# Optimization experiments

Measured on AMD Instinct MI355X. Metric: run time of the kernel, lower is better.

Reference implementation:

```python
import jax, jax.numpy as jnp
import numpy as np

NUM_NODES = 256
IN_FEAT = 64
HIDDEN = 512
N_CLASSES = 2
BATCH = 256


def setup_inputs() -> dict:
    key = jax.random.key(0)
    ks = jax.random.split(key, 10)
    return {
        "z": jax.random.normal(ks[0], (BATCH, 1, NUM_NODES, NUM_NODES), dtype=jnp.float32),
        "node_emb": jax.random.normal(ks[1], (NUM_NODES, IN_FEAT), dtype=jnp.float32),
        "w1": jax.random.normal(ks[2], (IN_FEAT, HIDDEN), dtype=jnp.float32) * (1.0 / np.sqrt(IN_FEAT)),
        "b1": jnp.zeros((HIDDEN,), dtype=jnp.float32),
        "w2": jax.random.normal(ks[3], (HIDDEN, HIDDEN), dtype=jnp.float32) * (1.0 / np.sqrt(HIDDEN)),
        "b2": jnp.zeros((HIDDEN,), dtype=jnp.float32),
        "w3": jax.random.normal(ks[4], (HIDDEN, HIDDEN), dtype=jnp.float32) * (1.0 / np.sqrt(HIDDEN)),
        "b3": jnp.zeros((HIDDEN,), dtype=jnp.float32),
        "fcw": jax.random.normal(ks[5], (HIDDEN, N_CLASSES), dtype=jnp.float32) * (1.0 / np.sqrt(HIDDEN)),
        "fcb": jnp.zeros((N_CLASSES,), dtype=jnp.float32),
    }


def reference(z, node_emb, w1, b1, w2, b2, w3, b3, fcw, fcb):
    # z: (B, 1, N, N) latent interpreted as weighted adjacency
    z_sq = jnp.squeeze(z, axis=1)                         # (B, N, N)
    A = jax.nn.sigmoid(z_sq)
    A = (A + jnp.swapaxes(A, 1, 2)) * 0.5                  # symmetrize
    A_hat = A + jnp.eye(A.shape[-1], dtype=A.dtype)[None]  # add self loops
    D_hat = jnp.sum(A_hat, axis=2) + 1e-6                  # (B, N) degrees
    d_inv_sqrt = D_hat ** -0.5
    # norm_A = D^{-1/2} A_hat D^{-1/2} via row/col scaling (same math as diag bmm)
    norm_A = A_hat * d_inv_sqrt[:, :, None] * d_inv_sqrt[:, None, :]

    X = jnp.broadcast_to(node_emb[None], (z.shape[0],) + node_emb.shape)  # (B, N, F)
    H1 = jax.nn.relu(jnp.einsum('bij,bjh->bih', norm_A, X @ w1 + b1))
    H2 = jax.nn.relu(jnp.einsum('bij,bjh->bih', norm_A, H1 @ w2 + b2))
    H3 = jax.nn.relu(jnp.einsum('bij,bjh->bih', norm_A, H2 @ w3 + b3))
    graph_emb = jnp.mean(H3, axis=1)                       # (B, H)
    logits = graph_emb @ fcw + fcb                         # (B, n_classes)
    return logits
```

## Files before the change

kernel.cpp:

```cpp
#include <hip/hip_runtime.h>
#include <stdint.h>

#define B_ 256
#define N_ 256
#define F_ 64
#define H_ 512

typedef _Float16 f16;
typedef _Float16 f16x8 __attribute__((ext_vector_type(8)));
typedef _Float16 f16x4 __attribute__((ext_vector_type(4)));
typedef _Float16 f16x2 __attribute__((ext_vector_type(2)));
typedef float    f32x4 __attribute__((ext_vector_type(4)));

__device__ __forceinline__ float sigmoidf_(float x) {
    return 1.0f / (1.0f + __expf(-x));
}

#define BAR_ACQ(N) do { \
    asm volatile("s_waitcnt vmcnt(" #N ")" ::: "memory"); \
    __builtin_amdgcn_s_barrier(); \
    __builtin_amdgcn_sched_barrier(0); } while (0)
#define BAR_REL() do { \
    __builtin_amdgcn_sched_barrier(0); \
    __builtin_amdgcn_s_barrier(); } while (0)

__global__ __launch_bounds__(512) void k_fsum(const float* __restrict__ z,
                                              f16* __restrict__ nA) {
    __shared__ f16 T[256 * 256];
    __shared__ float cpart[8][256];
    __shared__ float rpart[256][2];
    __shared__ float Dv[256];

    const int b = blockIdx.x;
    const int tid = threadIdx.x, lane = tid & 63, w = tid >> 6;
    const float* zb = z + (size_t)b * (N_ * N_);

    auto swz = [](int i) { return (i & 31) ^ (i >> 5); };

    float colacc[4] = {0.f, 0.f, 0.f, 0.f};
    const int ch = lane >> 1, half = lane & 1;
    for (int r = 0; r < 32; r++) {
        int i = w * 32 + r;
        float4 v = *(const float4*)(zb + (size_t)i * N_ + lane * 4);
        float s0 = sigmoidf_(v.x), s1 = sigmoidf_(v.y),
              s2 = sigmoidf_(v.z), s3 = sigmoidf_(v.w);
        f16x4 sv = { (f16)s0, (f16)s1, (f16)s2, (f16)s3 };
        *(f16x4*)&T[i * 256 + ((ch ^ swz(i)) << 3) + half * 4] = sv;
        colacc[0] += s0; colacc[1] += s1; colacc[2] += s2; colacc[3] += s3;
    }
    #pragma unroll
    for (int k = 0; k < 4; k++) cpart[w][lane * 4 + k] = colacc[k];
    __syncthreads();

    {
        int i = tid >> 1, h = tid & 1;
        float s = 0.f;
        #pragma unroll
        for (int c = 0; c < 16; c++) {
            int cc = h * 16 + c;
            f16x8 v = *(const f16x8*)&T[i * 256 + ((cc ^ swz(i)) << 3)];
            #pragma unroll
            for (int k = 0; k < 8; k++) s += (float)v[k];
        }
        rpart[i][h] = s;
    }
    __syncthreads();

    if (tid < 256) {
        float cs = 0.f;
        #pragma unroll
        for (int ww = 0; ww < 8; ww++) cs += cpart[ww][tid];
        float rs = rpart[tid][0] + rpart[tid][1];
        Dv[tid] = rsqrtf(1.0f + 1e-6f + 0.5f * (rs + cs));
    }
    __syncthreads();

    f16* Ob = nA + (size_t)b * (N_ * N_);
    #pragma unroll
    for (int tt = 0; tt < 2; tt++) {
        int tile = tt * 512 + tid;
        int I = tile >> 5, J = tile & 31;
        f16x8 a[8], bm[8];
        #pragma unroll
        for (int r = 0; r < 8; r++) {
            int ia = I * 8 + r;
            a[r] = *(const f16x8*)&T[ia * 256 + ((J ^ swz(ia)) << 3)];
        }
        #pragma unroll
        for (int r = 0; r < 8; r++) {
            int jb = J * 8 + r;
            bm[r] = *(const f16x8*)&T[jb * 256 + ((I ^ swz(jb)) << 3)];
        }
        float dj[8];
        #pragma unroll
        for (int k = 0; k < 8; k++) dj[k] = Dv[J * 8 + k];
        #pragma unroll
        for (int r = 0; r < 8; r++) {
            float di = Dv[I * 8 + r];
            f16x8 o;
            #pragma unroll
            for (int k = 0; k < 8; k++) {
                float v = 0.5f * ((float)a[r][k] + (float)bm[k][r]);
                if (I * 8 + r == J * 8 + k) v += 1.0f;
                o[k] = (f16)(v * di * dj[k]);
            }
            *(f16x8*)&Ob[(size_t)(I * 8 + r) * N_ + J * 8] = o;
        }
    }
}

__global__ __launch_bounds__(256) void k_prep(const float* __restrict__ ne,
                                              const float* __restrict__ w1,
                                              const float* __restrict__ b1,
                                              const float* __restrict__ w2,
                                              const float* __restrict__ w3,
                                              f16* __restrict__ XW1t,
                                              f16* __restrict__ w2t,
                                              f16* __restrict__ w3t) {
    int bid = blockIdx.x;
    if (bid < 512) {
        int h = bid, node = threadIdx.x;
        float s = b1[h];
        #pragma unroll 8
        for (int k = 0; k < F_; k++) s += ne[node * F_ + k] * w1[k * H_ + h];
        XW1t[h * N_ + node] = (f16)s;
    } else {
        int idx4 = bid - 512;
        int which = idx4 >> 10;
        const float* src = which ? w3 : w2;
        f16* dst = which ? w3t : w2t;
        int idx = (idx4 & 1023) * 256 + threadIdx.x;
        int k = idx >> 9, n = idx & 511;
        dst[n * H_ + k] = (f16)src[k * H_ + n];
    }
}

template <int KDIM, int MODE>
__global__ __launch_bounds__(256, 4) void k_gemm(const f16* __restrict__ A, long aBatch,
                                                 const f16* __restrict__ Bt, long bBatch,
                                                 f16* __restrict__ Out,
                                                 const float* __restrict__ bias,
                                                 float* __restrict__ gp) {
    __shared__ f16 As[128 * 64];
    __shared__ f16 Bs[128 * 64];
    const int tid  = threadIdx.x;
    const int lane = tid & 63, wave = tid >> 6;
    const int wm = wave >> 1, wn = wave & 1;

    const int lin = blockIdx.x;
    const int xcd = lin & 7, q = lin >> 3;
    const int n_t = q & 3, p = q >> 2;
    const int grp = xcd * 64 + p;
    const int b   = grp >> 1, m_t = grp & 1;
    const int m0 = m_t * 128, n0 = n_t * 128;

    const f16* Ab = A + (size_t)b * aBatch;
    const f16* Bb = Bt + (size_t)b * bBatch;

    f32x4 acc[4][4];
    #pragma unroll
    for (int i = 0; i < 4; i++)
        #pragma unroll
        for (int j = 0; j < 4; j++)
            #pragma unroll
            for (int r = 0; r < 4; r++) acc[i][j][r] = 0.0f;

    const int lr = lane >> 3;
    const int kc = (lane & 7) ^ lr;
    const int ln15 = lane & 15;

    for (int kk = 0; kk < KDIM; kk += 64) {
        #pragma unroll
        for (int c = 0; c < 4; c++) {
            int chunk = wave * 4 + c;
            int row = chunk * 8 + lr;
            __builtin_amdgcn_global_load_lds(
                (__attribute__((address_space(1))) void*)(Ab + (size_t)(m0 + row) * KDIM + kk + kc * 8),
                (__attribute__((address_space(3))) void*)(&As[chunk * 512]), 16, 0, 0);
            __builtin_amdgcn_global_load_lds(
                (__attribute__((address_space(1))) void*)(Bb + (size_t)(n0 + row) * KDIM + kk + kc * 8),
                (__attribute__((address_space(3))) void*)(&Bs[chunk * 512]), 16, 0, 0);
        }
        __syncthreads();

        #pragma unroll
        for (int ks = 0; ks < 2; ks++) {
            const int rkc = ks * 4 + (lane >> 4);
            f16x8 aF[4];
            #pragma unroll
            for (int t = 0; t < 4; t++) {
                int ra = wm * 64 + t * 16 + ln15;
                aF[t] = *(const f16x8*)&As[(ra * 8 + (rkc ^ (ra & 7))) * 8];
            }
            #pragma unroll
            for (int h2 = 0; h2 < 2; h2++) {
                f16x8 bF[2];
                #pragma unroll
                for (int t = 0; t < 2; t++) {
                    int rb = wn * 64 + (h2 * 2 + t) * 16 + ln15;
                    bF[t] = *(const f16x8*)&Bs[(rb * 8 + (rkc ^ (rb & 7))) * 8];
                }
                #pragma unroll
                for (int mt = 0; mt < 4; mt++)
                    #pragma unroll
                    for (int t = 0; t < 2; t++)
                        acc[mt][h2 * 2 + t] = __builtin_amdgcn_mfma_f32_16x16x32_f16(aF[mt], bF[t], acc[mt][h2 * 2 + t], 0, 0, 0);
            }
        }
        __syncthreads();
    }

    const int quad = lane >> 4;
    if (MODE == 0) {
        f16* Ob = Out + (size_t)b * (N_ * H_);
        #pragma unroll
        for (int mt = 0; mt < 4; mt++) {
            int node = m0 + wm * 64 + mt * 16 + quad * 4;
            #pragma unroll
            for (int nt = 0; nt < 4; nt++) {
                int h = n0 + wn * 64 + nt * 16 + ln15;
                #pragma unroll
                for (int rr = 0; rr < 4; rr++) {
                    float v = acc[mt][nt][rr];
                    v = v > 0.f ? v : 0.f;
                    Ob[(size_t)(node + rr) * H_ + h] = (f16)v;
                }
            }
        }
    }
}

template <int REDUCE>
__global__ __launch_bounds__(1024, 4) void k_fused(const f16* __restrict__ Hin,
                                                   const f16* __restrict__ Wt,
                                                   const float* __restrict__ bias,
                                                   const f16* __restrict__ nA,
                                                   f16* __restrict__ Hout,
                                                   float* __restrict__ gp) {
    __shared__ f16 As[2][16384];
    __shared__ f16 WU[32768];

    const int tid  = threadIdx.x;
    const int lane = tid & 63, wave = tid >> 6;
    const int ln15 = lane & 15, quad = lane >> 4;
    const int wm = wave >> 2, wn = wave & 3;

    const int lin = blockIdx.x;
    const int xcd = lin & 7, p = lin >> 3;
    const int grp = xcd * 128 + p;
    const int b = grp >> 2, hc = grp & 3;

    const f16* Hb = Hin + (size_t)b * (N_ * H_);
    const f16* Ab = nA + (size_t)b * (N_ * N_);
    const f16* Wc = Wt + (size_t)(hc * 128) * H_;

    const int lr = lane >> 3;
    const int kc = (lane & 7) ^ lr;

    auto stage1 = [&](int buf, int kt) {
        #pragma unroll
        for (int c = 0; c < 2; c++) {
            int chunk = wave * 2 + c;
            int row = chunk * 8 + lr;
            __builtin_amdgcn_global_load_lds(
                (__attribute__((address_space(1))) void*)(Hb + (size_t)row * H_ + kt * 64 + kc * 8),
                (__attribute__((address_space(3))) void*)(&As[buf][chunk * 512]), 16, 0, 0);
        }
        {
            int chunk = wave;
            int row = chunk * 8 + lr;
            __builtin_amdgcn_global_load_lds(
                (__attribute__((address_space(1))) void*)(Wc + (size_t)row * H_ + kt * 64 + kc * 8),
                (__attribute__((address_space(3))) void*)(&WU[buf * 8192 + chunk * 512]), 16, 0, 0);
        }
    };
    auto stage2 = [&](int buf, int jt) {
        #pragma unroll
        for (int c = 0; c < 2; c++) {
            int chunk = wave * 2 + c;
            int row = chunk * 8 + lr;
            __builtin_amdgcn_global_load_lds(
                (__attribute__((address_space(1))) void*)(Ab + (size_t)row * N_ + jt * 64 + kc * 8),
                (__attribute__((address_space(3))) void*)(&As[buf][chunk * 512]), 16, 0, 0);
        }
    };

    f32x4 acc[4][2];
    #pragma unroll
    for (int i = 0; i < 4; i++)
        #pragma unroll
        for (int j = 0; j < 2; j++)
            #pragma unroll
            for (int r = 0; r < 4; r++) acc[i][j][r] = 0.0f;

    stage1(0, 0);
    for (int kt = 0; kt < 8; ++kt) {
        const int buf = kt & 1;
        if (kt < 7) {
            stage1(buf ^ 1, kt + 1);
            BAR_ACQ(3);
        } else {
            stage2(0, 0);
            BAR_ACQ(2);
        }
        __builtin_amdgcn_s_setprio(1);
        #pragma unroll
        for (int ks = 0; ks < 2; ks++) {
            const int rkc = ks * 4 + quad;
            f16x8 aF[4], bF[2];
            #pragma unroll
            for (int t = 0; t < 4; t++) {
                int ra = wm * 64 + t * 16 + ln15;
                aF[t] = *(const f16x8*)&As[buf][(ra * 8 + (rkc ^ (ra & 7))) * 8];
            }
            #pragma unroll
            for (int t = 0; t < 2; t++) {
                int rb = wn * 32 + t * 16 + ln15;
                bF[t] = *(const f16x8*)&WU[buf * 8192 + (rb * 8 + (rkc ^ (rb & 7))) * 8];
            }
            #pragma unroll
            for (int mt = 0; mt < 4; mt++)
                #pragma unroll
                for (int nt = 0; nt < 2; nt++)
                    acc[mt][nt] = __builtin_amdgcn_mfma_f32_16x16x32_f16(aF[mt], bF[nt], acc[mt][nt], 0, 0, 0);
        }
        __builtin_amdgcn_s_setprio(0);
        BAR_REL();
    }

    #pragma unroll
    for (int nt = 0; nt < 2; nt++) {
        int hl = wn * 32 + nt * 16 + ln15;
        float bv = bias[hc * 128 + hl];
        #pragma unroll
        for (int mt = 0; mt < 4; mt++) {
            int j = wm * 64 + mt * 16 + quad * 4;
            int slot = (j >> 3) ^ (hl & 7);
            f16x4 v;
            #pragma unroll
            for (int rr = 0; rr < 4; rr++) v[rr] = (f16)(acc[mt][nt][rr] + bv);
            *(f16x4*)&WU[hl * 256 + slot * 8 + (j & 7)] = v;
        }
    }
    asm volatile("s_waitcnt lgkmcnt(0)" ::: "memory");
    __builtin_amdgcn_s_barrier();
    __builtin_amdgcn_sched_barrier(0);

    #pragma unroll
    for (int i = 0; i < 4; i++)
        #pragma unroll
        for (int j = 0; j < 2; j++)
            #pragma unroll
            for (int r = 0; r < 4; r++) acc[i][j][r] = 0.0f;

    for (int jt = 0; jt < 4; ++jt) {
        const int buf = jt & 1;
        if (jt < 3) {
            stage2(buf ^ 1, jt + 1);
            BAR_ACQ(2);
        } else {
            BAR_ACQ(0);
        }
        __builtin_amdgcn_s_setprio(1);
        #pragma unroll
        for (int ks = 0; ks < 2; ks++) {
            const int rkc = ks * 4 + quad;
            f16x8 aF[4], bF[2];
            #pragma unroll
            for (int t = 0; t < 4; t++) {
                int ra = wm * 64 + t * 16 + ln15;
                aF[t] = *(const f16x8*)&As[buf][(ra * 8 + (rkc ^ (ra & 7))) * 8];
            }
            #pragma unroll
            for (int t = 0; t < 2; t++) {
                int rb = wn * 32 + t * 16 + ln15;
                int g = jt * 8 + rkc;
                bF[t] = *(const f16x8*)&WU[rb * 256 + ((g ^ (rb & 7)) * 8)];
            }
            #pragma unroll
            for (int mt = 0; mt < 4; mt++)
                #pragma unroll
                for (int nt = 0; nt < 2; nt++)
                    acc[mt][nt] = __builtin_amdgcn_mfma_f32_16x16x32_f16(aF[mt], bF[nt], acc[mt][nt], 0, 0, 0);
        }
        __builtin_amdgcn_s_setprio(0);
        BAR_REL();
    }

    if (REDUCE == 0) {
        f16* Ob = Hout + (size_t)b * (N_ * H_);
        #pragma unroll
        for (int mt = 0; mt < 4; mt++) {
            int node = wm * 64 + mt * 16 + quad * 4;
            #pragma unroll
            for (int nt = 0; nt < 2; nt++) {
                int hg = hc * 128 + wn * 32 + nt * 16 + ln15;
                #pragma unroll
                for (int rr = 0; rr < 4; rr++) {
                    float v = acc[mt][nt][rr];
                    v = v > 0.f ? v : 0.f;
                    Ob[(size_t)(node + rr) * H_ + hg] = (f16)v;
                }
            }
        }
    } else {
        float part[2];
        #pragma unroll
        for (int nt = 0; nt < 2; nt++) {
            float s = 0.f;
            #pragma unroll
            for (int mt = 0; mt < 4; mt++)
                #pragma unroll
                for (int rr = 0; rr < 4; rr++) {
                    float v = acc[mt][nt][rr];
                    s += (v > 0.f ? v : 0.f);
                }
            s += __shfl_down(s, 32, 64);
            s += __shfl_down(s, 16, 64);
            part[nt] = s;
        }
        __syncthreads();
        float* red = (float*)&As[0][0];
        if (quad == 0) {
            #pragma unroll
            for (int nt = 0; nt < 2; nt++)
                red[wave * 32 + nt * 16 + ln15] = part[nt];
        }
        __syncthreads();
        if (tid < 128) {
            int wnl = tid >> 5, cl = tid & 31;
            float g = red[(0 * 4 + wnl) * 32 + cl] + red[(1 * 4 + wnl) * 32 + cl]
                    + red[(2 * 4 + wnl) * 32 + cl] + red[(3 * 4 + wnl) * 32 + cl];
            gp[(size_t)b * H_ + hc * 128 + tid] = g;
        }
    }
}

__global__ __launch_bounds__(256) void k_logits(const float* __restrict__ gp,
                                                const float* __restrict__ fcw,
                                                const float* __restrict__ fcb,
                                                float* __restrict__ out) {
    int b = blockIdx.x, tid = threadIdx.x;
    const float* g = gp + (size_t)b * H_;
    float g0 = g[tid];
    float g1 = g[tid + 256];
    float p0 = g0 * fcw[tid * 2 + 0] + g1 * fcw[(tid + 256) * 2 + 0];
    float p1 = g0 * fcw[tid * 2 + 1] + g1 * fcw[(tid + 256) * 2 + 1];
    for (int off = 32; off; off >>= 1) {
        p0 += __shfl_down(p0, off, 64);
        p1 += __shfl_down(p1, off, 64);
    }
    __shared__ float r0[4], r1[4];
    int lane = tid & 63, w = tid >> 6;
    if (lane == 0) { r0[w] = p0; r1[w] = p1; }
    __syncthreads();
    const float inv = 1.0f / N_;
    if (tid == 0) out[b * 2 + 0] = (r0[0] + r0[1] + r0[2] + r0[3]) * inv + fcb[0];
    if (tid == 1) out[b * 2 + 1] = (r1[0] + r1[1] + r1[2] + r1[3]) * inv + fcb[1];
}

extern "C" void kernel_launch(void* const* d_in, const int* in_sizes, int n_in,
                              void* d_out, int out_size, void* d_ws, size_t ws_size,
                              hipStream_t stream) {
    const float* z   = (const float*)d_in[0];
    const float* ne  = (const float*)d_in[1];
    const float* w1  = (const float*)d_in[2];
    const float* b1  = (const float*)d_in[3];
    const float* w2  = (const float*)d_in[4];
    const float* b2  = (const float*)d_in[5];
    const float* w3  = (const float*)d_in[6];
    const float* b3  = (const float*)d_in[7];
    const float* fcw = (const float*)d_in[8];
    const float* fcb = (const float*)d_in[9];
    float* out = (float*)d_out;

    char* ws = (char*)d_ws;
    f16*   T     = (f16*)(ws + 0);
    f16*   nA    = (f16*)(ws + 67108864);
    f16*   Hh    = (f16*)(ws + 100663296);
    float* gpart = (float*)(ws + 100663296);
    f16*   XW1t  = (f16*)(ws + 167772160);
    f16*   w2t   = (f16*)(ws + 168034304);
    f16*   w3t   = (f16*)(ws + 168558592);

    k_fsum<<<256, 512, 0, stream>>>(z, nA);
    k_prep<<<2560, 256, 0, stream>>>(ne, w1, b1, w2, w3, XW1t, w2t, w3t);

    k_gemm<256, 0><<<2048, 256, 0, stream>>>(nA, 65536, XW1t, 0, Hh, nullptr, nullptr);
    k_fused<0><<<1024, 1024, 0, stream>>>(Hh, w2t, b2, nA, T, nullptr);
    k_fused<1><<<1024, 1024, 0, stream>>>(T, w3t, b3, nA, nullptr, gpart);

    k_logits<<<B_, 256, 0, stream>>>(gpart, fcw, fcb, out);
}
```

Measured before the change: 293.2 us.

## Fuse first GCN aggregation GEMM into adjacency normalization kernel

The normalized adjacency is now written back into the block's shared-memory tile, and that tile is used directly as the A operand of an MFMA GEMM against XW1t to produce H1 within the same kernel. This removes the separate k_gemm launch and its re-read of nA from global memory. Normalization now runs over only the lower-triangular 8x8 tile pairs and writes each mirrored tile from registers, which halves the shared-memory loads. The tradeoffs are that k_prep must run before k_fsum, and that only 256 blocks of 512 threads perform the first layer's GEMM, with B fragments read straight from global memory and no staging.

Result: slower. 383.0 us (+30.6%).

```diff
diff --git a/kernel.cpp b/kernel.cpp
--- a/kernel.cpp
+++ b/kernel.cpp
@@ -25,7 +25,9 @@
     __builtin_amdgcn_s_barrier(); } while (0)
 
 __global__ __launch_bounds__(512) void k_fsum(const float* __restrict__ z,
-                                              f16* __restrict__ nA) {
+                                              const f16* __restrict__ XW1t,
+                                              f16* __restrict__ nA,
+                                              f16* __restrict__ H1) {
     __shared__ f16 T[256 * 256];
     __shared__ float cpart[8][256];
     __shared__ float rpart[256][2];
@@ -65,7 +67,6 @@
         rpart[i][h] = s;
     }
     __syncthreads();
-
     if (tid < 256) {
         float cs = 0.f;
         #pragma unroll
@@ -76,10 +77,14 @@
     __syncthreads();
 
     f16* Ob = nA + (size_t)b * (N_ * N_);
-    #pragma unroll
-    for (int tt = 0; tt < 2; tt++) {
-        int tile = tt * 512 + tid;
-        int I = tile >> 5, J = tile & 31;
+    for (int pp = 0; pp < 2; pp++) {
+        if (pp == 1 && tid >= 16) break;
+        int p = pp * 512 + tid;
+        int I = (int)((sqrtf(8.0f * (float)p + 1.0f) - 1.0f) * 0.5f);
+        while (I * (I + 1) / 2 > p) I--;
+        while ((I + 1) * (I + 2) / 2 <= p) I++;
+        int J = p - I * (I + 1) / 2;
+
         f16x8 a[8], bm[8];
         #pragma unroll
         for (int r = 0; r < 8; r++) {
@@ -91,20 +96,88 @@
             int jb = J * 8 + r;
             bm[r] = *(const f16x8*)&T[jb * 256 + ((I ^ swz(jb)) << 3)];
         }
-        float dj[8];
-        #pragma unroll
-        for (int k = 0; k < 8; k++) dj[k] = Dv[J * 8 + k];
+        float di[8], dj[8];
+        #pragma unroll
+        for (int k = 0; k < 8; k++) { di[k] = Dv[I * 8 + k]; dj[k] = Dv[J * 8 + k]; }
+
+        f16x8 o[8];
         #pragma unroll
         for (int r = 0; r < 8; r++) {
-            float di = Dv[I * 8 + r];
-            f16x8 o;
             #pragma unroll
             for (int k = 0; k < 8; k++) {
                 float v = 0.5f * ((float)a[r][k] + (float)bm[k][r]);
-                if (I * 8 + r == J * 8 + k) v += 1.0f;
-                o[k] = (f16)(v * di * dj[k]);
-            }
-            *(f16x8*)&Ob[(size_t)(I * 8 + r) * N_ + J * 8] = o;
+                if (I == J && r == k) v += 1.0f;
+                o[r][k] = (f16)(v * di[r] * dj[k]);
+            }
+        }
+        #pragma unroll
+        for (int r = 0; r < 8; r++) {
+            int ia = I * 8 + r;
+            *(f16x8*)&Ob[(size_t)ia * N_ + J * 8] = o[r];
+            *(f16x8*)&T[ia * 256 + ((J ^ swz(ia)) << 3)] = o[r];
+        }
+        if (I != J) {
+            #pragma unroll
+            for (int r = 0; r < 8; r++) {
+                int jb = J * 8 + r;
+                f16x8 om;
+                #pragma unroll
+                for (int k = 0; k < 8; k++) om[k] = o[k][r];
+                *(f16x8*)&Ob[(size_t)jb * N_ + I * 8] = om;
+                *(f16x8*)&T[jb * 256 + ((I ^ swz(jb)) << 3)] = om;
+            }
+        }
+    }
+    __syncthreads();
+
+    const int ln15 = lane & 15, quad = lane >> 4;
+    const int wm = w >> 1, wn = w & 1;
+    f16* Hb = H1 + (size_t)b * (N_ * H_);
+    for (int no = 0; no < 4; no++) {
+        const int n0 = (wn * 4 + no) * 64;
+        f32x4 acc[4][4];
+        #pragma unroll
+        for (int i = 0; i < 4; i++)
+            #pragma unroll
+            for (int j = 0; j < 4; j++)
+                #pragma unroll
+                for (int r = 0; r < 4; r++) acc[i][j][r] = 0.0f;
+
+        for (int kk = 0; kk < 4; kk++) {
+            #pragma unroll
+            for (int ks = 0; ks < 2; ks++) {
+                const int g = kk * 8 + ks * 4 + quad;
+                f16x8 aF[4], bF[4];
+                #pragma unroll
+                for (int t = 0; t < 4; t++) {
+                    int i = wm * 64 + t * 16 + ln15;
+                    aF[t] = *(const f16x8*)&T[i * 256 + ((g ^ swz(i)) << 3)];
+                }
+                #pragma unroll
+                for (int t = 0; t < 4; t++) {
+                    int h = n0 + t * 16 + ln15;
+                    bF[t] = *(const f16x8*)&XW1t[(size_t)h * 256 + g * 8];
+                }
+                #pragma unroll
+                for (int mt = 0; mt < 4; mt++)
+                    #pragma unroll
+                    for (int nt = 0; nt < 4; nt++)
+                        acc[mt][nt] = __builtin_amdgcn_mfma_f32_16x16x32_f16(aF[mt], bF[nt], acc[mt][nt], 0, 0, 0);
+            }
+        }
+        #pragma unroll
+        for (int mt = 0; mt < 4; mt++) {
+            int node = wm * 64 + mt * 16 + quad * 4;
+            #pragma unroll
+            for (int nt = 0; nt < 4; nt++) {
+                int h = n0 + nt * 16 + ln15;
+                #pragma unroll
+                for (int rr = 0; rr < 4; rr++) {
+                    float v = acc[mt][nt][rr];
+                    v = v > 0.f ? v : 0.f;
+                    Hb[(size_t)(node + rr) * H_ + h] = (f16)v;
+                }
+            }
         }
     }
 }
@@ -135,101 +208,6 @@
     }
 }
 
-template <int KDIM, int MODE>
-__global__ __launch_bounds__(256, 4) void k_gemm(const f16* __restrict__ A, long aBatch,
-                                                 const f16* __restrict__ Bt, long bBatch,
-                                                 f16* __restrict__ Out,
-                                                 const float* __restrict__ bias,
-                                                 float* __restrict__ gp) {
-    __shared__ f16 As[128 * 64];
-    __shared__ f16 Bs[128 * 64];
-    const int tid  = threadIdx.x;
-    const int lane = tid & 63, wave = tid >> 6;
-    const int wm = wave >> 1, wn = wave & 1;
-
-    const int lin = blockIdx.x;
-    const int xcd = lin & 7, q = lin >> 3;
-    const int n_t = q & 3, p = q >> 2;
-    const int grp = xcd * 64 + p;
-    const int b   = grp >> 1, m_t = grp & 1;
-    const int m0 = m_t * 128, n0 = n_t * 128;
-
-    const f16* Ab = A + (size_t)b * aBatch;
-    const f16* Bb = Bt + (size_t)b * bBatch;
-
-    f32x4 acc[4][4];
-    #pragma unroll
-    for (int i = 0; i < 4; i++)
-        #pragma unroll
-        for (int j = 0; j < 4; j++)
-            #pragma unroll
-            for (int r = 0; r < 4; r++) acc[i][j][r] = 0.0f;
-
-    const int lr = lane >> 3;
-    const int kc = (lane & 7) ^ lr;
-    const int ln15 = lane & 15;
-
-    for (int kk = 0; kk < KDIM; kk += 64) {
-        #pragma unroll
-        for (int c = 0; c < 4; c++) {
-            int chunk = wave * 4 + c;
-            int row = chunk * 8 + lr;
-            __builtin_amdgcn_global_load_lds(
-                (__attribute__((address_space(1))) void*)(Ab + (size_t)(m0 + row) * KDIM + kk + kc * 8),
-                (__attribute__((address_space(3))) void*)(&As[chunk * 512]), 16, 0, 0);
-            __builtin_amdgcn_global_load_lds(
-                (__attribute__((address_space(1))) void*)(Bb + (size_t)(n0 + row) * KDIM + kk + kc * 8),
-                (__attribute__((address_space(3))) void*)(&Bs[chunk * 512]), 16, 0, 0);
-        }
-        __syncthreads();
-
-        #pragma unroll
-        for (int ks = 0; ks < 2; ks++) {
-            const int rkc = ks * 4 + (lane >> 4);
-            f16x8 aF[4];
-            #pragma unroll
-            for (int t = 0; t < 4; t++) {
-                int ra = wm * 64 + t * 16 + ln15;
-                aF[t] = *(const f16x8*)&As[(ra * 8 + (rkc ^ (ra & 7))) * 8];
-            }
-            #pragma unroll
-            for (int h2 = 0; h2 < 2; h2++) {
-                f16x8 bF[2];
-                #pragma unroll
-                for (int t = 0; t < 2; t++) {
-                    int rb = wn * 64 + (h2 * 2 + t) * 16 + ln15;
-                    bF[t] = *(const f16x8*)&Bs[(rb * 8 + (rkc ^ (rb & 7))) * 8];
-                }
-                #pragma unroll
-                for (int mt = 0; mt < 4; mt++)
-                    #pragma unroll
-                    for (int t = 0; t < 2; t++)
-                        acc[mt][h2 * 2 + t] = __builtin_amdgcn_mfma_f32_16x16x32_f16(aF[mt], bF[t], acc[mt][h2 * 2 + t], 0, 0, 0);
-            }
-        }
-        __syncthreads();
-    }
-
-    const int quad = lane >> 4;
-    if (MODE == 0) {
-        f16* Ob = Out + (size_t)b * (N_ * H_);
-        #pragma unroll
-        for (int mt = 0; mt < 4; mt++) {
-            int node = m0 + wm * 64 + mt * 16 + quad * 4;
-            #pragma unroll
-            for (int nt = 0; nt < 4; nt++) {
-                int h = n0 + wn * 64 + nt * 16 + ln15;
-                #pragma unroll
-                for (int rr = 0; rr < 4; rr++) {
-                    float v = acc[mt][nt][rr];
-                    v = v > 0.f ? v : 0.f;
-                    Ob[(size_t)(node + rr) * H_ + h] = (f16)v;
-                }
-            }
-        }
-    }
-}
-
 template <int REDUCE>
 __global__ __launch_bounds__(1024, 4) void k_fused(const f16* __restrict__ Hin,
                                                    const f16* __restrict__ Wt,
@@ -483,10 +461,9 @@
     f16*   w2t   = (f16*)(ws + 168034304);
     f16*   w3t   = (f16*)(ws + 168558592);
 
-    k_fsum<<<256, 512, 0, stream>>>(z, nA);
     k_prep<<<2560, 256, 0, stream>>>(ne, w1, b1, w2, w3, XW1t, w2t, w3t);
-
-    k_gemm<256, 0><<<2048, 256, 0, stream>>>(nA, 65536, XW1t, 0, Hh, nullptr, nullptr);
+    k_fsum<<<256, 512, 0, stream>>>(z, XW1t, nA, Hh);
+
     k_fused<0><<<1024, 1024, 0, stream>>>(Hh, w2t, b2, nA, T, nullptr);
     k_fused<1><<<1024, 1024, 0, stream>>>(T, w3t, b3, nA, nullptr, gpart);
 
```

## Replace layer-1 GEMM with double-buffered 1024-thread kernel computing full hidden width

Applied to the files above, without the earlier changes.

The first aggregation GEMM (norm_A times XW1) is rewritten so each 1024-thread block handles one 128-node tile across all 512 hidden features in two passes. This replaces four 256-thread blocks that each reloaded the same A tile. Global-to-LDS loads are double-buffered with explicit waitcnt barriers and raised wave priority around the MFMA section. The operands are swapped so output writes become vectorized 4-wide f16 stores. The intent is to cut redundant A traffic and hide load latency, at the cost of fewer, larger blocks and more LDS per block.

Result: slower. 301.9 us (+3.0%).

```diff
diff --git a/kernel.cpp b/kernel.cpp
--- a/kernel.cpp
+++ b/kernel.cpp
@@ -135,99 +135,117 @@
     }
 }
 
-template <int KDIM, int MODE>
-__global__ __launch_bounds__(256, 4) void k_gemm(const f16* __restrict__ A, long aBatch,
-                                                 const f16* __restrict__ Bt, long bBatch,
-                                                 f16* __restrict__ Out,
-                                                 const float* __restrict__ bias,
-                                                 float* __restrict__ gp) {
-    __shared__ f16 As[128 * 64];
-    __shared__ f16 Bs[128 * 64];
-    const int tid  = threadIdx.x;
+__global__ __launch_bounds__(1024, 4) void k_gemm2(const f16* __restrict__ nA,
+                                                   const f16* __restrict__ XW1t,
+                                                   f16* __restrict__ H1) {
+    __shared__ f16 Bs[2][16384];
+    __shared__ f16 Am[2][8192];
+
+    const int tid = threadIdx.x;
     const int lane = tid & 63, wave = tid >> 6;
-    const int wm = wave >> 1, wn = wave & 1;
+    const int ln15 = lane & 15, quad = lane >> 4;
+    const int wm = wave >> 2, wn = wave & 3;
 
     const int lin = blockIdx.x;
-    const int xcd = lin & 7, q = lin >> 3;
-    const int n_t = q & 3, p = q >> 2;
+    const int xcd = lin & 7, p = lin >> 3;
     const int grp = xcd * 64 + p;
-    const int b   = grp >> 1, m_t = grp & 1;
-    const int m0 = m_t * 128, n0 = n_t * 128;
-
-    const f16* Ab = A + (size_t)b * aBatch;
-    const f16* Bb = Bt + (size_t)b * bBatch;
-
-    f32x4 acc[4][4];
+    const int b = grp >> 1, m_t = grp & 1;
+    const int m0 = m_t * 128;
+
+    const f16* Ab = nA + (size_t)b * (N_ * N_);
+    f16* Hb = H1 + (size_t)b * (N_ * H_);
+
+    const int lr = lane >> 3;
+    const int kc = (lane & 7) ^ lr;
+
+    auto stage = [&](int s) {
+        int pass = (s >> 2) & 1, kt = s & 3, buf = s & 1;
+        #pragma unroll
+        for (int c = 0; c < 2; c++) {
+            int chunk = wave * 2 + c;
+            int row = pass * 256 + chunk * 8 + lr;
+            __builtin_amdgcn_global_load_lds(
+                (__attribute__((address_space(1))) void*)(XW1t + (size_t)row * 256 + kt * 64 + kc * 8),
+                (__attribute__((address_space(3))) void*)(&Bs[buf][chunk * 512]), 16, 0, 0);
+        }
+        {
+            int chunk = wave;
+            int row = m0 + chunk * 8 + lr;
+            __builtin_amdgcn_global_load_lds(
+                (__attribute__((address_space(1))) void*)(Ab + (size_t)row * N_ + kt * 64 + kc * 8),
+                (__attribute__((address_space(3))) void*)(&Am[buf][chunk * 512]), 16, 0, 0);
+        }
+    };
+
+    f32x4 acc[4][2];
     #pragma unroll
     for (int i = 0; i < 4; i++)
         #pragma unroll
-        for (int j = 0; j < 4; j++)
+        for (int j = 0; j < 2; j++)
             #pragma unroll
             for (int r = 0; r < 4; r++) acc[i][j][r] = 0.0f;
 
-    const int lr = lane >> 3;
-    const int kc = (lane & 7) ^ lr;
-    const int ln15 = lane & 15;
-
-    for (int kk = 0; kk < KDIM; kk += 64) {
-        #pragma unroll
-        for (int c = 0; c < 4; c++) {
-            int chunk = wave * 4 + c;
-            int row = chunk * 8 + lr;
-            __builtin_amdgcn_global_load_lds(
-                (__attribute__((address_space(1))) void*)(Ab + (size_t)(m0 + row) * KDIM + kk + kc * 8),
-                (__attribute__((address_space(3))) void*)(&As[chunk * 512]), 16, 0, 0);
-            __builtin_amdgcn_global_load_lds(
-                (__attribute__((address_space(1))) void*)(Bb + (size_t)(n0 + row) * KDIM + kk + kc * 8),
-                (__attribute__((address_space(3))) void*)(&Bs[chunk * 512]), 16, 0, 0);
-        }
-        __syncthreads();
-
+    auto cwrite = [&](int pass) {
+        #pragma unroll
+        for (int mt = 0; mt < 4; mt++) {
+            int h0 = pass * 256 + wm * 64 + mt * 16 + quad * 4;
+            #pragma unroll
+            for (int nt = 0; nt < 2; nt++) {
+                int node = m0 + wn * 32 + nt * 16 + ln15;
+                f16x4 v;
+                #pragma unroll
+                for (int rr = 0; rr < 4; rr++) {
+                    float x = acc[mt][nt][rr];
+                    v[rr] = (f16)(x > 0.f ? x : 0.f);
+                }
+                *(f16x4*)&Hb[(size_t)node * H_ + h0] = v;
+            }
+        }
+    };
+
+    stage(0);
+    for (int s = 0; s < 8; ++s) {
+        const int buf = s & 1;
+        if (s < 7) {
+            stage(s + 1);
+            BAR_ACQ(3);
+        } else {
+            BAR_ACQ(0);
+        }
+        __builtin_amdgcn_s_setprio(1);
         #pragma unroll
         for (int ks = 0; ks < 2; ks++) {
-            const int rkc = ks * 4 + (lane >> 4);
-            f16x8 aF[4];
+            const int rkc = ks * 4 + quad;
+            f16x8 aF[4], bF[2];
             #pragma unroll
             for (int t = 0; t < 4; t++) {
                 int ra = wm * 64 + t * 16 + ln15;
-                aF[t] = *(const f16x8*)&As[(ra * 8 + (rkc ^ (ra & 7))) * 8];
-            }
-            #pragma unroll
-            for (int h2 = 0; h2 < 2; h2++) {
-                f16x8 bF[2];
-                #pragma unroll
-                for (int t = 0; t < 2; t++) {
-                    int rb = wn * 64 + (h2 * 2 + t) * 16 + ln15;
-                    bF[t] = *(const f16x8*)&Bs[(rb * 8 + (rkc ^ (rb & 7))) * 8];
-                }
-                #pragma unroll
-                for (int mt = 0; mt < 4; mt++)
+                aF[t] = *(const f16x8*)&Bs[buf][(ra * 8 + (rkc ^ (ra & 7))) * 8];
+            }
+            #pragma unroll
+            for (int t = 0; t < 2; t++) {
+                int rb = wn * 32 + t * 16 + ln15;
+                bF[t] = *(const f16x8*)&Am[buf][(rb * 8 + (rkc ^ (rb & 7))) * 8];
+            }
+            #pragma unroll
+            for (int mt = 0; mt < 4; mt++)
+                #pragma unroll
+                for (int nt = 0; nt < 2; nt++)
+                    acc[mt][nt] = __builtin_amdgcn_mfma_f32_16x16x32_f16(aF[mt], bF[nt], acc[mt][nt], 0, 0, 0);
+        }
+        __builtin_amdgcn_s_setprio(0);
+        if (s == 3) {
+            cwrite(0);
+            #pragma unroll
+            for (int i = 0; i < 4; i++)
+                #pragma unroll
+                for (int j = 0; j < 2; j++)
                     #pragma unroll
-                    for (int t = 0; t < 2; t++)
-                        acc[mt][h2 * 2 + t] = __builtin_amdgcn_mfma_f32_16x16x32_f16(aF[mt], bF[t], acc[mt][h2 * 2 + t], 0, 0, 0);
-            }
-        }
-        __syncthreads();
-    }
-
-    const int quad = lane >> 4;
-    if (MODE == 0) {
-        f16* Ob = Out + (size_t)b * (N_ * H_);
-        #pragma unroll
-        for (int mt = 0; mt < 4; mt++) {
-            int node = m0 + wm * 64 + mt * 16 + quad * 4;
-            #pragma unroll
-            for (int nt = 0; nt < 4; nt++) {
-                int h = n0 + wn * 64 + nt * 16 + ln15;
-                #pragma unroll
-                for (int rr = 0; rr < 4; rr++) {
-                    float v = acc[mt][nt][rr];
-                    v = v > 0.f ? v : 0.f;
-                    Ob[(size_t)(node + rr) * H_ + h] = (f16)v;
-                }
-            }
-        }
-    }
+                    for (int r = 0; r < 4; r++) acc[i][j][r] = 0.0f;
+        }
+        BAR_REL();
+    }
+    cwrite(1);
 }
 
 template <int REDUCE>
@@ -486,7 +504,7 @@
     k_fsum<<<256, 512, 0, stream>>>(z, nA);
     k_prep<<<2560, 256, 0, stream>>>(ne, w1, b1, w2, w3, XW1t, w2t, w3t);
 
-    k_gemm<256, 0><<<2048, 256, 0, stream>>>(nA, 65536, XW1t, 0, Hh, nullptr, nullptr);
+    k_gemm2<<<512, 1024, 0, stream>>>(nA, XW1t, Hh);
     k_fused<0><<<1024, 1024, 0, stream>>>(Hh, w2t, b2, nA, T, nullptr);
     k_fused<1><<<1024, 1024, 0, stream>>>(T, w3t, b3, nA, nullptr, gpart);
 
```
